# Kernel tuning notes

Hardware: AMD Instinct MI355X
Metric: run time of the kernel (lower is better)

## Reference

```python
import jax, jax.numpy as jnp
import numpy as np

EPS = 1e-15

def _layernorm(x, g, b, eps=1e-5):
    mu = x.mean(-1, keepdims=True)
    var = ((x - mu) ** 2).mean(-1, keepdims=True)
    return (x - mu) * jax.lax.rsqrt(var + eps) * g + b


def setup_inputs() -> dict:
    key = jax.random.key(0)
    ks = jax.random.split(key, 16)
    B, N, F, H, E, K, C, P, D = 2, 8192, 1024, 512, 512, 100, 2, 32, 1024
    g = lambda k, s: jax.random.normal(k, s, jnp.float32) * 0.02
    return {
        'node_feat': jax.random.normal(ks[0], (B, N, F), jnp.float32),
        'adj': jax.random.uniform(ks[1], (B, N, N), jnp.float32),
        'mask': jnp.ones((B, N), jnp.float32),
        'fc1_w': g(ks[2], (F, H)), 'fc1_b': jnp.zeros((H,), jnp.float32),
        'gcn_w': g(ks[3], (H, E)), 'gcn_b': jnp.zeros((E,), jnp.float32),
        'pool_w': g(ks[4], (E, K)), 'pool_b': jnp.zeros((K,), jnp.float32),
        'cls_token': jnp.zeros((1, 1, E), jnp.float32),
        'aw1': g(ks[5], (E, E)), 'ab1': jnp.zeros((E,), jnp.float32),
        'aw2': g(ks[6], (E, 1)), 'ab2': jnp.zeros((1,), jnp.float32),
        'pred_w': g(ks[7], (E, C)), 'pred_b': jnp.zeros((C,), jnp.float32),
        'gl_w': g(ks[8], (D, D)), 'gl_b': jnp.zeros((D,), jnp.float32),
        'gr_w': g(ks[9], (D, D)), 'gr_b': jnp.zeros((D,), jnp.float32),
        'ln_g': jnp.ones((D,), jnp.float32), 'ln_b': jnp.zeros((D,), jnp.float32),
        'protos_l': jax.random.normal(ks[10], (P, D), jnp.float32),
        'protos_r': jax.random.normal(ks[11], (P, D), jnp.float32),
    }


def reference(node_feat, adj, mask, fc1_w, fc1_b, gcn_w, gcn_b, pool_w, pool_b,
              cls_token, aw1, ab1, aw2, ab2, pred_w, pred_b,
              gl_w, gl_b, gr_w, gr_b, ln_g, ln_b, protos_l, protos_r):
    B = node_feat.shape[0]
    K = pool_w.shape[1]
    # _fc1: Linear + ReLU, then mask
    X = jax.nn.relu(node_feat @ fc1_w + fc1_b)
    X = mask[:, :, None] * X
    # GCNBlock: y = adj @ x (+ self), linear, L2-normalize along feature dim
    y = jnp.einsum('bnm,bmh->bnh', adj, X) + X  # add_self=1
    y = y @ gcn_w + gcn_b
    X = y / (jnp.linalg.norm(y, axis=2, keepdims=True) + 1e-12)  # F.normalize p=2 dim=2
    # pooling assignment
    s_raw = X @ pool_w + pool_b  # [B,N,K]
    # dense_mincut_pool
    s = jax.nn.softmax(s_raw, axis=-1) * mask[:, :, None]
    Xm = X * mask[:, :, None]
    out = jnp.einsum('bnk,bne->bke', s, Xm)                     # s^T x
    adj_s = jnp.einsum('bnm,bmk->bnk', adj, s)                  # adj @ s
    out_adj = jnp.einsum('bnk,bnl->bkl', s, adj_s)              # s^T adj s
    mincut_num = jnp.einsum('bnk,bnk->b', s, adj_s)             # trace(s^T A s)
    d_flat = adj.sum(-1)                                        # degrees
    mincut_den = jnp.einsum('bn,bnk,bnk->b', d_flat, s, s)      # trace(s^T D s)
    mincut_loss = -jnp.mean(mincut_num / (mincut_den + EPS))
    ss = jnp.einsum('bnk,bnl->bkl', s, s)
    i_s = jnp.eye(K, dtype=s.dtype)
    ss_fro = jnp.linalg.norm(ss, axis=(-2, -1), keepdims=True)
    ortho_loss = jnp.mean(jnp.linalg.norm(ss / (ss_fro + EPS) - i_s / jnp.sqrt(jnp.float32(K)), axis=(-2, -1)))
    # zero diagonal + symmetric degree normalization of pooled adjacency
    out_adj = out_adj * (1.0 - i_s)
    d = jnp.sqrt(out_adj.sum(-1)) + EPS
    out_adj = out_adj / d[:, :, None] / d[:, None, :]
    loss = mincut_loss + ortho_loss
    # cls token + per-cluster attention / instance logits
    Xp = jnp.concatenate([jnp.broadcast_to(cls_token, (B, 1, cls_token.shape[-1])), out], axis=1)  # [B,K+1,E]
    attn = jax.nn.sigmoid(jnp.tanh(Xp @ aw1 + ab1) @ aw2 + ab2)
    instance_logits = Xp @ pred_w + pred_b
    weighted_instance_logits = attn * instance_logits
    # CrossGatingFusion (tree prototype routing merge step)
    gate_l = jax.nn.sigmoid(protos_l @ gl_w + gl_b)
    gate_r = jax.nn.sigmoid(protos_r @ gr_w + gr_b)
    merged = _layernorm(gate_l * protos_l + gate_r * protos_r, ln_g, ln_b)
    return weighted_instance_logits, loss, merged, out_adj
```

## Files before the change

kernel.cpp:

```cpp
#include <hip/hip_runtime.h>

typedef unsigned short u16t;
typedef __bf16 bf16x8 __attribute__((ext_vector_type(8)));
typedef float floatx4 __attribute__((ext_vector_type(4)));
typedef u16t u16x8 __attribute__((ext_vector_type(8)));
typedef u16t u16x4 __attribute__((ext_vector_type(4)));

#define EPSF 1e-15f

__device__ __forceinline__ u16t f2bf(float f){
  unsigned u = __float_as_uint(f);
  u += 0x7fffu + ((u >> 16) & 1u);
  return (u16t)(u >> 16);
}
__device__ __forceinline__ float bf2f(u16t h){
  return __uint_as_float(((unsigned)h) << 16);
}

__device__ __forceinline__ float waveSum(float v){
  #pragma unroll
  for (int o = 32; o > 0; o >>= 1) v += __shfl_xor(v, o, 64);
  return v;
}
__device__ __forceinline__ float waveMax(float v){
  #pragma unroll
  for (int o = 32; o > 0; o >>= 1) v = fmaxf(v, __shfl_xor(v, o, 64));
  return v;
}
__device__ __forceinline__ float blockSum(float v, float* red){
  int lane = threadIdx.x & 63, w = threadIdx.x >> 6;
  v = waveSum(v);
  __syncthreads();
  if (lane == 0) red[w] = v;
  __syncthreads();
  float tot = 0.f;
  int nw = blockDim.x >> 6;
  for (int i = 0; i < nw; i++) tot += red[i];
  return tot;
}

template<bool SRCF32>
__global__ __launch_bounds__(256) void tr_k(const void* __restrict__ S, u16t* __restrict__ D,
    int M, int N, int lds_, int ldd, long long sS, long long sD)
{
  __shared__ u16t T[64][72];
  const int bz = blockIdx.z;
  const int r0 = blockIdx.y * 64, c0 = blockIdx.x * 64;
  const int t = threadIdx.x;
  const float* Sf = (const float*)S + (SRCF32 ? (size_t)bz * sS : 0);
  const u16t*  Sh = (const u16t*)S + (SRCF32 ? 0 : (size_t)bz * sS);
  #pragma unroll
  for (int p = 0; p < 2; p++){
    int row = p * 32 + (t >> 3), c8 = t & 7;
    int gr = r0 + row, gc = c0 + c8 * 8;
    u16x8 v = {0,0,0,0,0,0,0,0};
    if (gr < M){
      if constexpr (SRCF32){
        #pragma unroll
        for (int j = 0; j < 8; j++){
          int cc = gc + j;
          if (cc < N) v[j] = f2bf(Sf[(size_t)gr * lds_ + cc]);
        }
      } else {
        if (gc + 7 < N) v = *(const u16x8*)(Sh + (size_t)gr * lds_ + gc);
        else {
          #pragma unroll
          for (int j = 0; j < 8; j++){ int cc = gc + j; if (cc < N) v[j] = Sh[(size_t)gr * lds_ + cc]; }
        }
      }
    }
    *(u16x8*)(&T[row][c8 * 8]) = v;
  }
  __syncthreads();
  u16t* Db = D + (size_t)bz * sD;
  #pragma unroll
  for (int p = 0; p < 2; p++){
    int orow = p * 32 + (t >> 3), o8 = t & 7;
    int gc = c0 + orow;
    int gr = r0 + o8 * 8;
    if (gc < N){
      u16x8 v;
      #pragma unroll
      for (int j = 0; j < 8; j++) v[j] = T[o8 * 8 + j][orow];
      if (gr + 7 < M) *(u16x8*)(Db + (size_t)gc * ldd + gr) = v;
      else {
        #pragma unroll
        for (int j = 0; j < 8; j++) if (gr + j < M) Db[(size_t)gc * ldd + gr + j] = v[j];
      }
    }
  }
}

template<bool AF32, int EPI, bool DFLAT>
__global__ __launch_bounds__(256) void gemm_k(
    const void* __restrict__ Aptr, const u16t* __restrict__ Bt, void* __restrict__ Cptr,
    int M, int N, int K, int lda, int ldbt, int ldc,
    long long sA, long long sB, long long sC,
    const float* __restrict__ bias, int biasmax,
    const u16t* __restrict__ addsrc, int ldadd, long long sAdd,
    const float* __restrict__ mask,
    float* __restrict__ dflat,
    int nbx, int klen)
{
  __shared__ u16t As[128 * 40];
  __shared__ u16t Bs[128 * 40];
  const int bz = blockIdx.z;
  const int kc = blockIdx.x / nbx;
  const int bn0 = (blockIdx.x % nbx) * 128;
  const int bm0 = blockIdx.y * 128;
  const int t = threadIdx.x;
  const int lane = t & 63, wid = t >> 6;
  const int wm = wid >> 1, wn = wid & 1;
  const int l16 = lane & 15, quad = lane >> 4;
  const int kBeg = kc * klen;
  const int kEnd = (kBeg + klen < K) ? (kBeg + klen) : K;

  const float* Af = (const float*)Aptr + (AF32 ? (size_t)(bz * sA) : 0);
  const u16t*  Ah = (const u16t*)Aptr + (AF32 ? 0 : (size_t)(bz * sA));
  const u16t*  Bp = Bt + (size_t)(bz * sB);

  floatx4 acc[4][4];
  #pragma unroll
  for (int i = 0; i < 4; i++)
    #pragma unroll
    for (int j = 0; j < 4; j++)
      #pragma unroll
      for (int rg = 0; rg < 4; rg++) acc[i][j][rg] = 0.f;

  float dsum = 0.f;

  float4 afv[4];
  u16x8 ahv[2];
  u16x8 bhv[2];

  auto loadA = [&](int k0){
    if constexpr (AF32){
      #pragma unroll
      for (int i = 0; i < 4; i++){
        int c = t + i * 256;
        int r = c >> 3, c4 = c & 7;
        int gr = bm0 + r;
        afv[i] = make_float4(0.f, 0.f, 0.f, 0.f);
        if (gr < M) afv[i] = *(const float4*)(Af + (size_t)gr * lda + k0 + c4 * 4);
      }
    } else {
      #pragma unroll
      for (int i = 0; i < 2; i++){
        int c = t + i * 256;
        int r = c >> 2, c8 = c & 3;
        int gr = bm0 + r;
        ahv[i] = (u16x8){0,0,0,0,0,0,0,0};
        if (gr < M) ahv[i] = *(const u16x8*)(Ah + (size_t)gr * lda + k0 + c8 * 8);
      }
    }
  };
  auto loadB = [&](int k0){
    #pragma unroll
    for (int i = 0; i < 2; i++){
      int c = t + i * 256;
      int n = c >> 2, c8 = c & 3;
      int gc = bn0 + n;
      bhv[i] = (u16x8){0,0,0,0,0,0,0,0};
      if (gc < N) bhv[i] = *(const u16x8*)(Bp + (size_t)gc * ldbt + k0 + c8 * 8);
    }
  };
  auto storeTiles = [&](){
    if constexpr (AF32){
      #pragma unroll
      for (int i = 0; i < 4; i++){
        int c = t + i * 256;
        int r = c >> 3, c4 = c & 7;
        u16x4 hv;
        hv[0] = f2bf(afv[i].x); hv[1] = f2bf(afv[i].y);
        hv[2] = f2bf(afv[i].z); hv[3] = f2bf(afv[i].w);
        *(u16x4*)(&As[r * 40 + c4 * 4]) = hv;
      }
    } else {
      #pragma unroll
      for (int i = 0; i < 2; i++){
        int c = t + i * 256;
        int r = c >> 2, c8 = c & 3;
        *(u16x8*)(&As[r * 40 + c8 * 8]) = ahv[i];
      }
    }
    #pragma unroll
    for (int i = 0; i < 2; i++){
      int c = t + i * 256;
      int n = c >> 2, c8 = c & 3;
      *(u16x8*)(&Bs[n * 40 + c8 * 8]) = bhv[i];
    }
  };

  loadA(kBeg); loadB(kBeg);

  for (int k0 = kBeg; k0 < kEnd; k0 += 32){
    __syncthreads();
    storeTiles();
    __syncthreads();
    if (k0 + 32 < kEnd){ loadA(k0 + 32); loadB(k0 + 32); }
    if constexpr (DFLAT){
      int r = t >> 1, half = t & 1;
      float s = 0.f;
      #pragma unroll
      for (int q = 0; q < 16; q++) s += bf2f(As[r * 40 + half * 16 + q]);
      dsum += s;
    }
    u16x8 a[4], b[4];
    #pragma unroll
    for (int i = 0; i < 4; i++) a[i] = *(const u16x8*)(&As[(wm * 64 + i * 16 + l16) * 40 + quad * 8]);
    #pragma unroll
    for (int j = 0; j < 4; j++) b[j] = *(const u16x8*)(&Bs[(wn * 64 + j * 16 + l16) * 40 + quad * 8]);
    #pragma unroll
    for (int i = 0; i < 4; i++)
      #pragma unroll
      for (int j = 0; j < 4; j++)
        acc[i][j] = __builtin_amdgcn_mfma_f32_16x16x32_bf16(
            __builtin_bit_cast(bf16x8, a[i]), __builtin_bit_cast(bf16x8, b[j]),
            acc[i][j], 0, 0, 0);
  }

  if constexpr (DFLAT){
    float other = __shfl_xor(dsum, 1, 64);
    if ((t & 1) == 0){
      int gr = bm0 + (t >> 1);
      if (gr < M) atomicAdd(&dflat[(size_t)bz * 8192 + gr], dsum + other);
    }
  }

  float* Cf = (float*)Cptr + (size_t)(bz * sC);
  u16t*  Ch = (u16t*)Cptr + (size_t)(bz * sC);
  const u16t* addp = (EPI == 3) ? (addsrc + (size_t)(bz * sAdd)) : nullptr;
  #pragma unroll
  for (int i = 0; i < 4; i++){
    int rb = bm0 + wm * 64 + i * 16 + quad * 4;
    #pragma unroll
    for (int j = 0; j < 4; j++){
      int col = bn0 + wn * 64 + j * 16 + l16;
      if (col >= N) continue;
      float bv = bias ? bias[col > biasmax ? biasmax : col] : 0.f;
      #pragma unroll
      for (int rg = 0; rg < 4; rg++){
        int row = rb + rg;
        if (row >= M) continue;
        float v = acc[i][j][rg] + bv;
        if constexpr (EPI == 1){
          v = fmaxf(v, 0.f) * mask[row];
          Ch[(size_t)row * ldc + col] = f2bf(v);
        } else if constexpr (EPI == 2){
          Ch[(size_t)row * ldc + col] = f2bf(v);
        } else if constexpr (EPI == 3){
          v += bf2f(addp[(size_t)row * ldadd + col]);
          Cf[(size_t)row * ldc + col] = v;
        } else if constexpr (EPI == 4){
          atomicAdd(&Cf[(size_t)row * ldc + col], v);
        } else {
          Cf[(size_t)row * ldc + col] = v;
        }
      }
    }
  }
}

__global__ __launch_bounds__(256) void norm_k(const float* __restrict__ Z, u16t* __restrict__ CC){
  __shared__ float red[8];
  int n = blockIdx.x, t = threadIdx.x;
  const float* z = Z + (size_t)n * 512;
  float v0 = z[t], v1 = z[t + 256];
  float tot = blockSum(v0 * v0 + v1 * v1, red);
  float inv = 1.f / (sqrtf(tot) + 1e-12f);
  u16t* o = CC + (size_t)n * 768;
  o[t] = f2bf(v0 * inv);
  o[t + 256] = f2bf(v1 * inv);
}

__global__ __launch_bounds__(256) void softmax_k(const float* __restrict__ SR, const float* __restrict__ pb,
                                                 const float* __restrict__ mask,
                                                 u16t* __restrict__ CC, u16t* __restrict__ ST){
  int w = threadIdx.x >> 6, lane = threadIdx.x & 63;
  int n = blockIdx.x * 4 + w;
  const float* r = SR + (size_t)n * 112;
  float v0 = (lane < 100) ? r[lane] + pb[lane] : -1e30f;
  float v1 = (lane + 64 < 100) ? r[lane + 64] + pb[lane + 64] : -1e30f;
  float m = waveMax(fmaxf(v0, v1));
  float e0 = (lane < 100) ? __expf(v0 - m) : 0.f;
  float e1 = (lane + 64 < 100) ? __expf(v1 - m) : 0.f;
  float s = waveSum(e0 + e1);
  float inv = mask[n] / s;
  int b = n >> 13, nn = n & 8191;
  u16t* cc = CC + (size_t)n * 768 + 624;
  if (lane < 100){
    u16t h = f2bf(e0 * inv);
    cc[lane] = h;
    ST[((size_t)b * 112 + lane) * 8192 + nn] = h;
  }
  if (lane + 64 < 100){
    u16t h = f2bf(e1 * inv);
    cc[lane + 64] = h;
    ST[((size_t)b * 112 + lane + 64) * 8192 + nn] = h;
  }
}

__global__ void cvty3_k(const float* __restrict__ Y, u16t* __restrict__ CC){
  int n = blockIdx.x, t = threadIdx.x;
  if (t < 100) CC[(size_t)n * 768 + 512 + t] = f2bf(Y[(size_t)n * 112 + t]);
}

__global__ __launch_bounds__(256) void den_k(const u16t* __restrict__ CC, const float* __restrict__ dflat,
                                             float* __restrict__ scal){
  __shared__ float red[8];
  int n = blockIdx.x * 256 + threadIdx.x;
  const u16t* s = CC + (size_t)n * 768 + 624;
  float ssq = 0.f;
  for (int k = 0; k < 100; k++){ float v = bf2f(s[k]); ssq += v * v; }
  float tot = blockSum(dflat[n] * ssq, red);
  if (threadIdx.x == 0) atomicAdd(&scal[n >> 13], tot);
}

__global__ __launch_bounds__(256) void losses_k(const float* __restrict__ OUTB, const float* __restrict__ scal,
                                                float* __restrict__ dout){
  __shared__ float red[8];
  __shared__ float fro[2], orth[2], num[2];
  int t = threadIdx.x;
  for (int b = 0; b < 2; b++){
    const float* base = OUTB + (size_t)b * 112 * 768;
    float p = 0.f;
    for (int idx = t; idx < 10000; idx += 256){
      int k = idx / 100, l = idx - k * 100;
      float v = base[(size_t)k * 768 + 624 + l];
      p += v * v;
    }
    float tot = blockSum(p, red);
    if (t == 0) fro[b] = sqrtf(tot);
    float q = (t < 100) ? base[(size_t)t * 768 + 512 + t] : 0.f;
    float ntot = blockSum(q, red);
    if (t == 0) num[b] = ntot;
  }
  __syncthreads();
  for (int b = 0; b < 2; b++){
    const float* base = OUTB + (size_t)b * 112 * 768;
    float f = fro[b] + EPSF;
    float p = 0.f;
    for (int idx = t; idx < 10000; idx += 256){
      int k = idx / 100, l = idx - k * 100;
      float v = base[(size_t)k * 768 + 624 + l] / f - ((k == l) ? 0.1f : 0.f);
      p += v * v;
    }
    float tot = blockSum(p, red);
    if (t == 0) orth[b] = sqrtf(tot);
  }
  __syncthreads();
  if (t == 0){
    float mc = -0.5f * (num[0] / (scal[0] + EPSF) + num[1] / (scal[1] + EPSF));
    float ol = 0.5f * (orth[0] + orth[1]);
    dout[404] = mc + ol;
  }
}

__global__ __launch_bounds__(256) void outadj_k(const float* __restrict__ OUTB, float* __restrict__ dout){
  __shared__ float T[10000];
  __shared__ float D[100];
  int b = blockIdx.x, t = threadIdx.x;
  const float* base = OUTB + (size_t)b * 112 * 768;
  for (int idx = t; idx < 10000; idx += 256){
    int k = idx / 100, l = idx - k * 100;
    T[idx] = (k == l) ? 0.f : base[(size_t)k * 768 + 512 + l];
  }
  __syncthreads();
  if (t < 100){
    float s = 0.f;
    for (int l = 0; l < 100; l++) s += T[t * 100 + l];
    D[t] = sqrtf(s) + EPSF;
  }
  __syncthreads();
  float* o = dout + 33173 + b * 10000;
  for (int idx = t; idx < 10000; idx += 256){
    int k = idx / 100, l = idx - k * 100;
    o[idx] = T[idx] / (D[k] * D[l]);
  }
}

__global__ __launch_bounds__(256) void attn_k(const float* __restrict__ OUTB, const float* __restrict__ cls,
    const float* __restrict__ aw1, const float* __restrict__ ab1,
    const float* __restrict__ aw2, const float* __restrict__ ab2,
    const float* __restrict__ pw, const float* __restrict__ pb, float* __restrict__ dout){
  __shared__ float xp[512];
  __shared__ float h[512];
  __shared__ float red[8];
  int blk = blockIdx.x;
  int b = blk / 101, r = blk % 101;
  int t = threadIdx.x;
  const float* src = (r == 0) ? cls : (OUTB + ((size_t)b * 112 + (r - 1)) * 768);
  xp[t] = src[t]; xp[t + 256] = src[t + 256];
  __syncthreads();
  #pragma unroll
  for (int ee = 0; ee < 2; ee++){
    int e = t + ee * 256;
    float acc = ab1[e];
    for (int f = 0; f < 512; f++) acc += xp[f] * aw1[(size_t)f * 512 + e];
    h[e] = tanhf(acc);
  }
  __syncthreads();
  float pa = h[t] * aw2[t] + h[t + 256] * aw2[t + 256];
  float alog = blockSum(pa, red);
  float attn = 1.f / (1.f + __expf(-(alog + ab2[0])));
  float p0 = xp[t] * pw[(size_t)t * 2] + xp[t + 256] * pw[(size_t)(t + 256) * 2];
  float l0 = blockSum(p0, red);
  float p1 = xp[t] * pw[(size_t)t * 2 + 1] + xp[t + 256] * pw[(size_t)(t + 256) * 2 + 1];
  float l1 = blockSum(p1, red);
  if (t == 0){
    dout[((size_t)b * 101 + r) * 2 + 0] = attn * (l0 + pb[0]);
    dout[((size_t)b * 101 + r) * 2 + 1] = attn * (l1 + pb[1]);
  }
}

__global__ __launch_bounds__(256) void fusion_k(const float* __restrict__ PL, const float* __restrict__ PR,
    const float* __restrict__ GLW, const float* __restrict__ GLB,
    const float* __restrict__ GRW, const float* __restrict__ GRB,
    const float* __restrict__ LG, const float* __restrict__ LB, float* __restrict__ dout){
  __shared__ float pl[1024], pr[1024], pre[1024];
  __shared__ float red[8];
  int p = blockIdx.x, t = threadIdx.x;
  #pragma unroll
  for (int i = 0; i < 4; i++){
    pl[t + i * 256] = PL[(size_t)p * 1024 + t + i * 256];
    pr[t + i * 256] = PR[(size_t)p * 1024 + t + i * 256];
  }
  __syncthreads();
  #pragma unroll
  for (int i = 0; i < 4; i++){
    int j = t + i * 256;
    float al = GLB[j], ar = GRB[j];
    for (int d = 0; d < 1024; d++){
      al += pl[d] * GLW[(size_t)d * 1024 + j];
      ar += pr[d] * GRW[(size_t)d * 1024 + j];
    }
    float gl = 1.f / (1.f + __expf(-al));
    float gr = 1.f / (1.f + __expf(-ar));
    pre[j] = gl * pl[j] + gr * pr[j];
  }
  __syncthreads();
  float ps = 0.f;
  for (int i = 0; i < 4; i++) ps += pre[t + i * 256];
  float mu = blockSum(ps, red) * (1.f / 1024.f);
  float pv = 0.f;
  for (int i = 0; i < 4; i++){ float d = pre[t + i * 256] - mu; pv += d * d; }
  float var = blockSum(pv, red) * (1.f / 1024.f);
  float rs = rsqrtf(var + 1e-5f);
  float* o = dout + 405 + (size_t)p * 1024;
  for (int i = 0; i < 4; i++){
    int j = t + i * 256;
    o[j] = (pre[j] - mu) * rs * LG[j] + LB[j];
  }
}

extern "C" void kernel_launch(void* const* d_in, const int* in_sizes, int n_in,
                              void* d_out, int out_size, void* d_ws, size_t ws_size,
                              hipStream_t stream)
{
  const float* node_feat = (const float*)d_in[0];
  const float* adj   = (const float*)d_in[1];
  const float* maskp = (const float*)d_in[2];
  const float* fc1w  = (const float*)d_in[3];
  const float* fc1b  = (const float*)d_in[4];
  const float* gcnw  = (const float*)d_in[5];
  const float* gcnb  = (const float*)d_in[6];
  const float* poolw = (const float*)d_in[7];
  const float* poolb = (const float*)d_in[8];
  const float* cls   = (const float*)d_in[9];
  const float* aw1   = (const float*)d_in[10];
  const float* ab1   = (const float*)d_in[11];
  const float* aw2   = (const float*)d_in[12];
  const float* ab2   = (const float*)d_in[13];
  const float* predw = (const float*)d_in[14];
  const float* predb = (const float*)d_in[15];
  const float* glw   = (const float*)d_in[16];
  const float* glb   = (const float*)d_in[17];
  const float* grw   = (const float*)d_in[18];
  const float* grb   = (const float*)d_in[19];
  const float* lng   = (const float*)d_in[20];
  const float* lnb   = (const float*)d_in[21];
  const float* prl   = (const float*)d_in[22];
  const float* prr   = (const float*)d_in[23];
  float* dout = (float*)d_out;

  char* ws = (char*)d_ws;
  size_t off = 0;
  auto take = [&](size_t bytes) -> char* {
    char* p = ws + off;
    off = (off + bytes + 255) & ~(size_t)255;
    return p;
  };
  u16t* FC1WT = (u16t*)take((size_t)512 * 1024 * 2);
  u16t* GCNWT = (u16t*)take((size_t)512 * 512 * 2);
  u16t* POOLWT= (u16t*)take((size_t)100 * 512 * 2);
  u16t* X1    = (u16t*)take((size_t)16384 * 512 * 2);
  u16t* W     = (u16t*)take((size_t)16384 * 512 * 2);
  u16t* WT    = (u16t*)take((size_t)2 * 512 * 8192 * 2);
  float* Z    = (float*)take((size_t)16384 * 512 * 4);
  u16t* CC    = (u16t*)take((size_t)2 * 8192 * 768 * 2);
  u16t* CCT   = (u16t*)take((size_t)2 * 768 * 8192 * 2);
  u16t* ST    = (u16t*)take((size_t)2 * 112 * 8192 * 2);
  float* OUTB = (float*)take((size_t)2 * 112 * 768 * 4);
  float* Y3F  = (float*)take((size_t)16384 * 112 * 4);
  float* SRAW = (float*)take((size_t)16384 * 112 * 4);
  float* DFLAT= (float*)take((size_t)16384 * 4);
  float* SCAL = (float*)take(256);

  hipMemsetAsync(SCAL, 0, 32, stream);
  hipMemsetAsync(DFLAT, 0, (size_t)16384 * 4, stream);
  hipMemsetAsync(Y3F, 0, (size_t)16384 * 112 * 4, stream);
  hipMemsetAsync(SRAW, 0, (size_t)16384 * 112 * 4, stream);
  hipMemsetAsync(OUTB, 0, (size_t)2 * 112 * 768 * 4, stream);

  tr_k<true><<<dim3(8, 16, 1), 256, 0, stream>>>(fc1w, FC1WT, 1024, 512, 512, 1024, 0, 0);
  tr_k<true><<<dim3(8, 8, 1), 256, 0, stream>>>(gcnw, GCNWT, 512, 512, 512, 512, 0, 0);
  tr_k<true><<<dim3(2, 8, 1), 256, 0, stream>>>(poolw, POOLWT, 512, 100, 100, 512, 0, 0);

  gemm_k<true, 1, false><<<dim3(4, 128, 1), 256, 0, stream>>>(
      node_feat, FC1WT, X1, 16384, 512, 1024, 1024, 1024, 512,
      0, 0, 0, fc1b, 511, nullptr, 0, 0, maskp, nullptr, 4, 1024);
  gemm_k<false, 2, false><<<dim3(4, 128, 1), 256, 0, stream>>>(
      X1, GCNWT, W, 16384, 512, 512, 512, 512, 512,
      0, 0, 0, nullptr, 0, nullptr, 0, 0, nullptr, nullptr, 4, 512);
  tr_k<false><<<dim3(8, 128, 2), 256, 0, stream>>>(
      W, WT, 8192, 512, 512, 8192, (long long)8192 * 512, (long long)512 * 8192);
  gemm_k<true, 3, false><<<dim3(4, 64, 2), 256, 0, stream>>>(
      adj, WT, Z, 8192, 512, 8192, 8192, 8192, 512,
      (long long)8192 * 8192, (long long)512 * 8192, (long long)8192 * 512,
      gcnb, 511, W, 512, (long long)8192 * 512, nullptr, nullptr, 4, 8192);
  norm_k<<<16384, 256, 0, stream>>>(Z, CC);
  gemm_k<false, 4, false><<<dim3(2, 128, 1), 256, 0, stream>>>(
      CC, POOLWT, SRAW, 16384, 100, 512, 768, 512, 112,
      0, 0, 0, nullptr, 0, nullptr, 0, 0, nullptr, nullptr, 1, 256);
  softmax_k<<<4096, 256, 0, stream>>>(SRAW, poolb, maskp, CC, ST);
  gemm_k<true, 4, true><<<dim3(4, 64, 2), 256, 0, stream>>>(
      adj, ST, Y3F, 8192, 100, 8192, 8192, 8192, 112,
      (long long)8192 * 8192, (long long)112 * 8192, (long long)8192 * 112,
      nullptr, 0, nullptr, 0, 0, nullptr, DFLAT, 1, 2048);
  cvty3_k<<<16384, 128, 0, stream>>>(Y3F, CC);
  tr_k<false><<<dim3(12, 128, 2), 256, 0, stream>>>(
      CC, CCT, 8192, 768, 768, 8192, (long long)8192 * 768, (long long)768 * 8192);
  gemm_k<false, 4, false><<<dim3(96, 1, 2), 256, 0, stream>>>(
      ST, CCT, OUTB, 100, 736, 8192, 8192, 8192, 768,
      (long long)112 * 8192, (long long)768 * 8192, (long long)112 * 768,
      nullptr, 0, nullptr, 0, 0, nullptr, nullptr, 6, 512);

  den_k<<<64, 256, 0, stream>>>(CC, DFLAT, SCAL);
  losses_k<<<1, 256, 0, stream>>>(OUTB, SCAL, dout);
  outadj_k<<<2, 256, 0, stream>>>(OUTB, dout);
  attn_k<<<202, 256, 0, stream>>>(OUTB, cls, aw1, ab1, aw2, ab2, predw, predb, dout);
  fusion_k<<<32, 256, 0, stream>>>(prl, prr, glw, glb, grw, grb, lng, lnb, dout);

  (void)in_sizes; (void)n_in; (void)out_size; (void)ws_size;
}
```

Before: 1.797 ms.

## Pre-convert adjacency to bf16 once and reuse it in both adjacency GEMMs

Adds a pass that converts the fp32 adjacency matrix to bf16 once, computing its row sums (the degree) along the way. Both adjacency GEMMs then read the half-size bf16 copy instead of converting fp32 on the fly twice. The first of these GEMMs becomes split-K with atomic accumulation, and its bias and self-add move into a new normalize kernel. Other changes pad the LDS row stride from 40 to 44 to reduce bank conflicts, and increase the split-K count of the final pooling GEMM. The price is an extra 256MB workspace buffer, an added conversion pass over adj, and more atomics.

Result: slower. 1.890 ms (+5.2%).

```diff
diff --git a/kernel.cpp b/kernel.cpp
--- a/kernel.cpp
+++ b/kernel.cpp
@@ -7,6 +7,7 @@
 typedef u16t u16x4 __attribute__((ext_vector_type(4)));
 
 #define EPSF 1e-15f
+#define LDSP 44
 
 __device__ __forceinline__ u16t f2bf(float f){
   unsigned u = __float_as_uint(f);
@@ -37,6 +38,29 @@
   int nw = blockDim.x >> 6;
   for (int i = 0; i < nw; i++) tot += red[i];
   return tot;
+}
+
+__global__ __launch_bounds__(256) void cvtadj_k(const float* __restrict__ A, u16t* __restrict__ H,
+                                                float* __restrict__ dflat){
+  __shared__ float red[8];
+  size_t row = blockIdx.x;
+  const float* src = A + row * 8192;
+  u16t* dst = H + row * 8192;
+  int t = threadIdx.x;
+  float s = 0.f;
+  #pragma unroll
+  for (int i = 0; i < 4; i++){
+    int idx = i * 256 + t;
+    const float4 v0 = *(const float4*)(src + (size_t)idx * 8);
+    const float4 v1 = *(const float4*)(src + (size_t)idx * 8 + 4);
+    s += v0.x + v0.y + v0.z + v0.w + v1.x + v1.y + v1.z + v1.w;
+    u16x8 h;
+    h[0] = f2bf(v0.x); h[1] = f2bf(v0.y); h[2] = f2bf(v0.z); h[3] = f2bf(v0.w);
+    h[4] = f2bf(v1.x); h[5] = f2bf(v1.y); h[6] = f2bf(v1.z); h[7] = f2bf(v1.w);
+    *(u16x8*)(dst + (size_t)idx * 8) = h;
+  }
+  float tot = blockSum(s, red);
+  if (t == 0) dflat[row] = tot;
 }
 
 template<bool SRCF32>
@@ -102,8 +126,8 @@
     float* __restrict__ dflat,
     int nbx, int klen)
 {
-  __shared__ u16t As[128 * 40];
-  __shared__ u16t Bs[128 * 40];
+  __shared__ u16t As[128 * LDSP];
+  __shared__ u16t Bs[128 * LDSP];
   const int bz = blockIdx.z;
   const int kc = blockIdx.x / nbx;
   const int bn0 = (blockIdx.x % nbx) * 128;
@@ -173,21 +197,21 @@
         u16x4 hv;
         hv[0] = f2bf(afv[i].x); hv[1] = f2bf(afv[i].y);
         hv[2] = f2bf(afv[i].z); hv[3] = f2bf(afv[i].w);
-        *(u16x4*)(&As[r * 40 + c4 * 4]) = hv;
+        *(u16x4*)(&As[r * LDSP + c4 * 4]) = hv;
       }
     } else {
       #pragma unroll
       for (int i = 0; i < 2; i++){
         int c = t + i * 256;
         int r = c >> 2, c8 = c & 3;
-        *(u16x8*)(&As[r * 40 + c8 * 8]) = ahv[i];
+        *(u16x8*)(&As[r * LDSP + c8 * 8]) = ahv[i];
       }
     }
     #pragma unroll
     for (int i = 0; i < 2; i++){
       int c = t + i * 256;
       int n = c >> 2, c8 = c & 3;
-      *(u16x8*)(&Bs[n * 40 + c8 * 8]) = bhv[i];
+      *(u16x8*)(&Bs[n * LDSP + c8 * 8]) = bhv[i];
     }
   };
 
@@ -202,14 +226,14 @@
       int r = t >> 1, half = t & 1;
       float s = 0.f;
       #pragma unroll
-      for (int q = 0; q < 16; q++) s += bf2f(As[r * 40 + half * 16 + q]);
+      for (int q = 0; q < 16; q++) s += bf2f(As[r * LDSP + half * 16 + q]);
       dsum += s;
     }
     u16x8 a[4], b[4];
     #pragma unroll
-    for (int i = 0; i < 4; i++) a[i] = *(const u16x8*)(&As[(wm * 64 + i * 16 + l16) * 40 + quad * 8]);
+    for (int i = 0; i < 4; i++) a[i] = *(const u16x8*)(&As[(wm * 64 + i * 16 + l16) * LDSP + quad * 8]);
     #pragma unroll
-    for (int j = 0; j < 4; j++) b[j] = *(const u16x8*)(&Bs[(wn * 64 + j * 16 + l16) * 40 + quad * 8]);
+    for (int j = 0; j < 4; j++) b[j] = *(const u16x8*)(&Bs[(wn * 64 + j * 16 + l16) * LDSP + quad * 8]);
     #pragma unroll
     for (int i = 0; i < 4; i++)
       #pragma unroll
@@ -259,6 +283,21 @@
       }
     }
   }
+}
+
+__global__ __launch_bounds__(256) void norm2_k(const float* __restrict__ Z, const u16t* __restrict__ W,
+                                               const float* __restrict__ gb, u16t* __restrict__ CC){
+  __shared__ float red[8];
+  int n = blockIdx.x, t = threadIdx.x;
+  const float* z = Z + (size_t)n * 512;
+  const u16t* w = W + (size_t)n * 512;
+  float v0 = z[t] + bf2f(w[t]) + gb[t];
+  float v1 = z[t + 256] + bf2f(w[t + 256]) + gb[t + 256];
+  float tot = blockSum(v0 * v0 + v1 * v1, red);
+  float inv = 1.f / (sqrtf(tot) + 1e-12f);
+  u16t* o = CC + (size_t)n * 768;
+  o[t] = f2bf(v0 * inv);
+  o[t + 256] = f2bf(v1 * inv);
 }
 
 __global__ __launch_bounds__(256) void norm_k(const float* __restrict__ Z, u16t* __restrict__ CC){
@@ -505,16 +544,22 @@
   float* SRAW = (float*)take((size_t)16384 * 112 * 4);
   float* DFLAT= (float*)take((size_t)16384 * 4);
   float* SCAL = (float*)take(256);
+  u16t* ADJH  = (u16t*)take((size_t)2 * 8192 * 8192 * 2);
+  const bool big = (off <= ws_size);
 
   hipMemsetAsync(SCAL, 0, 32, stream);
-  hipMemsetAsync(DFLAT, 0, (size_t)16384 * 4, stream);
   hipMemsetAsync(Y3F, 0, (size_t)16384 * 112 * 4, stream);
   hipMemsetAsync(SRAW, 0, (size_t)16384 * 112 * 4, stream);
   hipMemsetAsync(OUTB, 0, (size_t)2 * 112 * 768 * 4, stream);
+  if (big) hipMemsetAsync(Z, 0, (size_t)16384 * 512 * 4, stream);
+  else     hipMemsetAsync(DFLAT, 0, (size_t)16384 * 4, stream);
 
   tr_k<true><<<dim3(8, 16, 1), 256, 0, stream>>>(fc1w, FC1WT, 1024, 512, 512, 1024, 0, 0);
   tr_k<true><<<dim3(8, 8, 1), 256, 0, stream>>>(gcnw, GCNWT, 512, 512, 512, 512, 0, 0);
   tr_k<true><<<dim3(2, 8, 1), 256, 0, stream>>>(poolw, POOLWT, 512, 100, 100, 512, 0, 0);
+
+  if (big)
+    cvtadj_k<<<16384, 256, 0, stream>>>(adj, ADJH, DFLAT);
 
   gemm_k<true, 1, false><<<dim3(4, 128, 1), 256, 0, stream>>>(
       node_feat, FC1WT, X1, 16384, 512, 1024, 1024, 1024, 512,
@@ -524,26 +569,44 @@
       0, 0, 0, nullptr, 0, nullptr, 0, 0, nullptr, nullptr, 4, 512);
   tr_k<false><<<dim3(8, 128, 2), 256, 0, stream>>>(
       W, WT, 8192, 512, 512, 8192, (long long)8192 * 512, (long long)512 * 8192);
-  gemm_k<true, 3, false><<<dim3(4, 64, 2), 256, 0, stream>>>(
-      adj, WT, Z, 8192, 512, 8192, 8192, 8192, 512,
-      (long long)8192 * 8192, (long long)512 * 8192, (long long)8192 * 512,
-      gcnb, 511, W, 512, (long long)8192 * 512, nullptr, nullptr, 4, 8192);
-  norm_k<<<16384, 256, 0, stream>>>(Z, CC);
+
+  if (big){
+    gemm_k<false, 4, false><<<dim3(8, 64, 2), 256, 0, stream>>>(
+        ADJH, WT, Z, 8192, 512, 8192, 8192, 8192, 512,
+        (long long)8192 * 8192, (long long)512 * 8192, (long long)8192 * 512,
+        nullptr, 0, nullptr, 0, 0, nullptr, nullptr, 4, 4096);
+    norm2_k<<<16384, 256, 0, stream>>>(Z, W, gcnb, CC);
+  } else {
+    gemm_k<true, 3, false><<<dim3(4, 64, 2), 256, 0, stream>>>(
+        adj, WT, Z, 8192, 512, 8192, 8192, 8192, 512,
+        (long long)8192 * 8192, (long long)512 * 8192, (long long)8192 * 512,
+        gcnb, 511, W, 512, (long long)8192 * 512, nullptr, nullptr, 4, 8192);
+    norm_k<<<16384, 256, 0, stream>>>(Z, CC);
+  }
+
   gemm_k<false, 4, false><<<dim3(2, 128, 1), 256, 0, stream>>>(
       CC, POOLWT, SRAW, 16384, 100, 512, 768, 512, 112,
       0, 0, 0, nullptr, 0, nullptr, 0, 0, nullptr, nullptr, 1, 256);
   softmax_k<<<4096, 256, 0, stream>>>(SRAW, poolb, maskp, CC, ST);
-  gemm_k<true, 4, true><<<dim3(4, 64, 2), 256, 0, stream>>>(
-      adj, ST, Y3F, 8192, 100, 8192, 8192, 8192, 112,
-      (long long)8192 * 8192, (long long)112 * 8192, (long long)8192 * 112,
-      nullptr, 0, nullptr, 0, 0, nullptr, DFLAT, 1, 2048);
+
+  if (big){
+    gemm_k<false, 4, false><<<dim3(8, 64, 2), 256, 0, stream>>>(
+        ADJH, ST, Y3F, 8192, 100, 8192, 8192, 8192, 112,
+        (long long)8192 * 8192, (long long)112 * 8192, (long long)8192 * 112,
+        nullptr, 0, nullptr, 0, 0, nullptr, nullptr, 1, 1024);
+  } else {
+    gemm_k<true, 4, true><<<dim3(4, 64, 2), 256, 0, stream>>>(
+        adj, ST, Y3F, 8192, 100, 8192, 8192, 8192, 112,
+        (long long)8192 * 8192, (long long)112 * 8192, (long long)8192 * 112,
+        nullptr, 0, nullptr, 0, 0, nullptr, DFLAT, 1, 2048);
+  }
   cvty3_k<<<16384, 128, 0, stream>>>(Y3F, CC);
   tr_k<false><<<dim3(12, 128, 2), 256, 0, stream>>>(
       CC, CCT, 8192, 768, 768, 8192, (long long)8192 * 768, (long long)768 * 8192);
-  gemm_k<false, 4, false><<<dim3(96, 1, 2), 256, 0, stream>>>(
+  gemm_k<false, 4, false><<<dim3(192, 1, 2), 256, 0, stream>>>(
       ST, CCT, OUTB, 100, 736, 8192, 8192, 8192, 768,
       (long long)112 * 8192, (long long)768 * 8192, (long long)112 * 768,
-      nullptr, 0, nullptr, 0, 0, nullptr, nullptr, 6, 512);
+      nullptr, 0, nullptr, 0, 0, nullptr, nullptr, 6, 256);
 
   den_k<<<64, 256, 0, stream>>>(CC, DFLAT, SCAL);
   losses_k<<<1, 256, 0, stream>>>(OUTB, SCAL, dout);
@@ -551,5 +614,5 @@
   attn_k<<<202, 256, 0, stream>>>(OUTB, cls, aw1, ab1, aw2, ab2, predw, predb, dout);
   fusion_k<<<32, 256, 0, stream>>>(prl, prr, glw, glb, grw, grb, lng, lnb, dout);
 
-  (void)in_sizes; (void)n_in; (void)out_size; (void)ws_size;
-}
+  (void)in_sizes; (void)n_in; (void)out_size;
+}
```
